# Kernel tuning notes

Measured on AMD Instinct MI355X. Metric: run time of the kernel, lower is better.

Reference implementation:

```python
import jax, jax.numpy as jnp
import numpy as np

EMBED_DIM = 1024
NUM_HEADS = 16
HEAD_DIM = EMBED_DIM // NUM_HEADS
GLOBAL_HEADS = 1
LOCAL_K = 128
SCALE = HEAD_DIM ** -0.5


def setup_inputs() -> dict:
    key = jax.random.key(0)
    ks = jax.random.split(key, 9)
    B, n = 4, 2048
    s = 1.0 / np.sqrt(EMBED_DIM)  # torch Linear default uniform(-1/sqrt(in), 1/sqrt(in))
    def lin(k):
        kw, kb = jax.random.split(k)
        W = jax.random.uniform(kw, (EMBED_DIM, EMBED_DIM), jnp.float32, -s, s)
        b = jax.random.uniform(kb, (EMBED_DIM,), jnp.float32, -s, s)
        return W, b
    wq, bq = lin(ks[0])
    wk, bk = lin(ks[1])
    wv, bv = lin(ks[2])
    wo, bo = lin(ks[3])
    x = jax.random.normal(ks[4], (B, n, EMBED_DIM), jnp.float32)
    return {"x": x, "wq": wq, "bq": bq, "wk": wk, "bk": bk,
            "wv": wv, "bv": bv, "wo": wo, "bo": bo}


def _attend(x, wq, bq, wk, bk, wv, bv, wo, bo):
    B, n, E = x.shape
    H, D = NUM_HEADS, HEAD_DIM
    def proj(W, b):
        t = x @ W.T + b                       # [B, n, E]
        return t.reshape(B, n, H, D).transpose(0, 2, 1, 3)  # [B, H, n, D]
    q, k, v = proj(wq, bq), proj(wk, bk), proj(wv, bv)
    scores = jnp.einsum('bhqd,bhkd->bhqk', q, k) * SCALE  # [B, H, n, n]
    idx = jnp.arange(n)
    band = jnp.abs(idx[:, None] - idx[None, :]) <= LOCAL_K  # [n, n] True = allowed
    is_global = jnp.arange(H) < GLOBAL_HEADS
    mask = band[None, :, :] | is_global[:, None, None]      # [H, n, n]
    scores = jnp.where(mask[None], scores, -jnp.inf)
    attn = jax.nn.softmax(scores, axis=-1)   # dropout is identity (p=0 / eval)
    out = jnp.einsum('bhqk,bhkd->bhqd', attn, v)
    out = out.transpose(0, 2, 1, 3).reshape(B, n, E)
    return out @ wo.T + bo


def reference(x, wq, bq, wk, bk, wv, bv, wo, bo):
    return _attend(x, wq, bq, wk, bk, wv, bv, wo, bo)
```

## Files before the change

kernel.cpp:

```cpp
#include <hip/hip_runtime.h>

typedef __attribute__((ext_vector_type(4))) float f32x4;
typedef __attribute__((ext_vector_type(8))) short s16x8;

#define GLDS(gsrc, ldst) \
  __builtin_amdgcn_global_load_lds((const __attribute__((address_space(1))) void*)(gsrc), \
                                   (__attribute__((address_space(3))) void*)(ldst), 16, 0, 0)

__device__ __forceinline__ ushort f2bf(float f) {
  union { float f; unsigned u; } x; x.f = f;
  unsigned r = (x.u + 0x7FFFu + ((x.u >> 16) & 1u)) >> 16;
  return (ushort)r;
}

__global__ __launch_bounds__(256) void castk(const float* __restrict__ in,
                                             ushort* __restrict__ outp, int n) {
  int i = (blockIdx.x * 256 + threadIdx.x) * 4;
  if (i >= n) return;
  float4 v = *(const float4*)(in + i);
  ushort4 r;
  r.x = f2bf(v.x); r.y = f2bf(v.y); r.z = f2bf(v.z); r.w = f2bf(v.w);
  *(ushort4*)(outp + i) = r;
}

__global__ __launch_bounds__(256) void castw(const float* __restrict__ w0, const float* __restrict__ w1,
                                             const float* __restrict__ w2, const float* __restrict__ w3,
                                             ushort* __restrict__ o0, ushort* __restrict__ o1,
                                             ushort* __restrict__ o2, ushort* __restrict__ o3) {
  int bid = blockIdx.x;
  int sel = bid >> 10;
  const float* in = (sel == 0) ? w0 : (sel == 1) ? w1 : (sel == 2) ? w2 : w3;
  ushort* outp    = (sel == 0) ? o0 : (sel == 1) ? o1 : (sel == 2) ? o2 : o3;
  int i = ((bid & 1023) * 256 + threadIdx.x) * 4;
  float4 v = *(const float4*)(in + i);
  ushort4 r;
  r.x = f2bf(v.x); r.y = f2bf(v.y); r.z = f2bf(v.z); r.w = f2bf(v.w);
  *(ushort4*)(outp + i) = r;
}

template<int OUTBF16>
__global__ __launch_bounds__(512, 2) void gemm256(
    const ushort* __restrict__ A, const ushort* __restrict__ Bt,
    const float* __restrict__ bias0, const float* __restrict__ bias1,
    const float* __restrict__ bias2,
    void* __restrict__ Cout, int M, int N, int K, int nxn)
{
  __shared__ __align__(16) ushort lds[73728];
  const int tid = threadIdx.x;
  const int w = tid >> 6, lane = tid & 63;
  const int lrow = lane & 15, lg = lane >> 4;
  const int wm = w >> 2, wn = w & 3;
  const int cpx = gridDim.x >> 3;
  const int wgid = ((int)blockIdx.x & 7) * cpx + ((int)blockIdx.x >> 3);
  const int mblk = (wgid / nxn) * 128;
  const int nblk = (wgid % nxn) * 256;
  const int NT = K >> 6;

  const int srow = tid >> 3;
  const int scol = 8 * ((tid & 7) ^ (srow & 7));
  const ushort* Abase = A + (size_t)(mblk + srow) * K + scol;
  const ushort* Bbase = Bt + (size_t)(nblk + srow) * K + scol;
  const size_t rstep = (size_t)64 * K;
  const int dA = w * 512;
  const int dB = 8192 + w * 512;

#define STAGE_A(kt, bf) { \
    GLDS(Abase + (size_t)(kt) * 64,         &lds[(bf) * 24576 + dA]); \
    GLDS(Abase + (size_t)(kt) * 64 + rstep, &lds[(bf) * 24576 + dA + 4096]); }
#define STAGE_B(kt, bf) { \
    GLDS(Bbase + (size_t)(kt) * 64,             &lds[(bf) * 24576 + dB]); \
    GLDS(Bbase + (size_t)(kt) * 64 + rstep,     &lds[(bf) * 24576 + dB + 4096]); \
    GLDS(Bbase + (size_t)(kt) * 64 + 2 * rstep, &lds[(bf) * 24576 + dB + 8192]); \
    GLDS(Bbase + (size_t)(kt) * 64 + 3 * rstep, &lds[(bf) * 24576 + dB + 12288]); }

  int offA[4][2], offB[4][2];
#pragma unroll
  for (int m = 0; m < 4; m++)
#pragma unroll
    for (int kk = 0; kk < 2; kk++) {
      offA[m][kk] = (wm * 64 + m * 16 + lrow) * 64 + (((kk * 4 + lg) ^ (lrow & 7)) << 3);
      offB[m][kk] = 8192 + (wn * 64 + m * 16 + lrow) * 64 + (((kk * 4 + lg) ^ (lrow & 7)) << 3);
    }

  const f32x4 zero = {0.f, 0.f, 0.f, 0.f};
  f32x4 acc[4][4];
#pragma unroll
  for (int m = 0; m < 4; m++)
#pragma unroll
    for (int n = 0; n < 4; n++) acc[m][n] = zero;

  STAGE_A(0, 0); STAGE_B(0, 0);
  if (NT > 1) { STAGE_A(1, 1); STAGE_B(1, 1); }

  int b = 0;
  for (int t = 0; t < NT; ++t) {
    if (t < NT - 1) { asm volatile("s_waitcnt vmcnt(6)" ::: "memory"); }
    else            { asm volatile("s_waitcnt vmcnt(0)" ::: "memory"); }
    __builtin_amdgcn_s_barrier();
    const int bb = b * 24576;
    const int t2 = t + 2;
    const int b2 = (b >= 1) ? b - 1 : 2;

    if (t2 < NT) STAGE_A(t2, b2);
    {
      s16x8 af[4], bf_[4];
#pragma unroll
      for (int m = 0; m < 4; m++) af[m] = *(const s16x8*)&lds[bb + offA[m][0]];
#pragma unroll
      for (int n = 0; n < 4; n++) bf_[n] = *(const s16x8*)&lds[bb + offB[n][0]];
      __builtin_amdgcn_s_setprio(1);
#pragma unroll
      for (int m = 0; m < 4; m++)
#pragma unroll
        for (int n = 0; n < 4; n++)
          acc[m][n] = __builtin_amdgcn_mfma_f32_16x16x32_bf16(af[m], bf_[n], acc[m][n], 0, 0, 0);
      __builtin_amdgcn_s_setprio(0);
    }
    if (t2 < NT) STAGE_B(t2, b2);
    {
      s16x8 af[4], bf_[4];
#pragma unroll
      for (int m = 0; m < 4; m++) af[m] = *(const s16x8*)&lds[bb + offA[m][1]];
#pragma unroll
      for (int n = 0; n < 4; n++) bf_[n] = *(const s16x8*)&lds[bb + offB[n][1]];
      __builtin_amdgcn_s_setprio(1);
#pragma unroll
      for (int m = 0; m < 4; m++)
#pragma unroll
        for (int n = 0; n < 4; n++)
          acc[m][n] = __builtin_amdgcn_mfma_f32_16x16x32_bf16(af[m], bf_[n], acc[m][n], 0, 0, 0);
      __builtin_amdgcn_s_setprio(0);
    }
    b = (b == 2) ? 0 : b + 1;
  }
#undef STAGE_A
#undef STAGE_B

  float bias_n[4];
#pragma unroll
  for (int n = 0; n < 4; n++) {
    const int col = nblk + wn * 64 + n * 16 + lrow;
    if (bias1) bias_n[n] = (col < 1024) ? bias0[col]
                          : (col < 2048 ? bias1[col - 1024] : bias2[col - 2048]);
    else bias_n[n] = bias0[col];
  }

  __syncthreads();

  if (OUTBF16) {
    ushort* Ct = lds;
#pragma unroll
    for (int m = 0; m < 4; m++)
#pragma unroll
      for (int n = 0; n < 4; n++)
#pragma unroll
        for (int i = 0; i < 4; i++)
          Ct[(wm * 64 + m * 16 + 4 * lg + i) * 256 + wn * 64 + n * 16 + lrow] =
              f2bf(acc[m][n][i] + bias_n[n]);
    __syncthreads();
    ushort* Cg = (ushort*)Cout;
#pragma unroll
    for (int r = 0; r < 8; r++) {
      const int row = r * 16 + (tid >> 5);
      const int col = (tid & 31) * 8;
      *(s16x8*)&Cg[(size_t)(mblk + row) * N + nblk + col] = *(const s16x8*)&lds[r * 4096 + tid * 8];
    }
  } else {
    float* Cf = (float*)lds;
#pragma unroll
    for (int m = 0; m < 4; m++)
#pragma unroll
      for (int n = 0; n < 4; n++)
#pragma unroll
        for (int i = 0; i < 4; i++)
          Cf[(wm * 64 + m * 16 + 4 * lg + i) * 256 + wn * 64 + n * 16 + lrow] =
              acc[m][n][i] + bias_n[n];
    __syncthreads();
    float* Cg = (float*)Cout;
#pragma unroll
    for (int r = 0; r < 16; r++) {
      const int row = r * 8 + (tid >> 6);
      const int col = (tid & 63) * 4;
      *(float4*)&Cg[(size_t)(mblk + row) * N + nblk + col] = *(const float4*)&Cf[r * 2048 + tid * 4];
    }
  }
}

__global__ __launch_bounds__(256) void attn_kernel(const ushort* __restrict__ qkv,
                                                   ushort* __restrict__ outp,
                                                   float* __restrict__ oPart,
                                                   float* __restrict__ mPart,
                                                   float* __restrict__ lPart)
{
  __shared__ __align__(16) ushort Ks[64 * 64];
  __shared__ __align__(16) ushort Vt[64 * 64];
  __shared__ __align__(16) ushort Ps[4][16 * 40];

  const int tid = threadIdx.x;
  const int w = tid >> 6, lane = tid & 63;
  const int lrow = lane & 15, lg = lane >> 4;

  const int bid = (blockIdx.x & 7) * 368 + (blockIdx.x >> 3);
  int h, b, bx, kv_lo, kv_hi, chunk = 0;
  bool isGlobal;
  if (bid < 1024) {
    isGlobal = true; h = 0;
    chunk = bid >> 7;
    int qb = bid & 127;
    b = qb >> 5; bx = qb & 31;
    kv_lo = chunk * 256; kv_hi = kv_lo + 256;
  } else {
    isGlobal = false;
    int t = bid - 1024;
    h = 1 + (t >> 7);
    int qb = t & 127;
    b = qb >> 5; bx = qb & 31;
    kv_lo = bx * 64 - 128; if (kv_lo < 0) kv_lo = 0;
    kv_hi = bx * 64 + 192; if (kv_hi > 2048) kv_hi = 2048;
  }
  const int q0b = bx * 64;
  const int q0 = q0b + w * 16;
  const ushort* Qp = qkv + (size_t)b * 2048 * 3072 + h * 64;
  const ushort* Kp = Qp + 1024;
  const ushort* Vp = Qp + 2048;

  s16x8 qf0 = *(const s16x8*)(Qp + (size_t)(q0 + lrow) * 3072 + 8 * lg);
  s16x8 qf1 = *(const s16x8*)(Qp + (size_t)(q0 + lrow) * 3072 + 32 + 8 * lg);

  const f32x4 zero = {0.f, 0.f, 0.f, 0.f};
  f32x4 o[4];
  o[0] = zero; o[1] = zero; o[2] = zero; o[3] = zero;
  float mrun = -3e38f, lsum = 0.f;
  const int q_abs = q0 + lrow;
  const float SCL = 0.18033688011112042f;

  const int sp = tid >> 3;
  const int sg = tid & 7;
  const int kr0 = tid >> 3;
  const int kc = tid & 7;
  const int vx = (lrow & 7) ^ (lrow >> 3);

  for (int kv = kv_lo; kv < kv_hi; kv += 64) {
    const bool needMask = !isGlobal && (kv < q0b - 64 || kv + 64 > q0b + 128);

    const ushort* vrow = Vp + (size_t)(kv + 2 * sp) * 3072 + 8 * sg;
    s16x8 vlo = *(const s16x8*)vrow;
    s16x8 vhi = *(const s16x8*)(vrow + 3072);

    __syncthreads();

    GLDS(Kp + (size_t)(kv + kr0) * 3072 + 8 * (kc ^ (kr0 & 7)), &Ks[w * 512]);
    GLDS(Kp + (size_t)(kv + 32 + kr0) * 3072 + 8 * (kc ^ (kr0 & 7)), &Ks[2048 + w * 512]);

#pragma unroll
    for (int j = 0; j < 8; j++) {
      const int d = 8 * sg + j;
      const int r = 2 * sp;
      uint pk = (uint)(ushort)vlo[j] | ((uint)(ushort)vhi[j] << 16);
      *(uint*)&Vt[d * 64 + ((((r >> 3) ^ j ^ sg) & 7) << 3) + (r & 7)] = pk;
    }
    __syncthreads();

#pragma unroll
    for (int s = 0; s < 2; s++) {
      const int kb = kv + 32 * s;
      const int rs = 32 * s;
      s16x8 kA0 = *(const s16x8*)&Ks[(rs + lrow) * 64      + ((( lg      ^ (lrow & 7)) & 7) << 3)];
      s16x8 kA1 = *(const s16x8*)&Ks[(rs + lrow) * 64      + ((((4 + lg) ^ (lrow & 7)) & 7) << 3)];
      s16x8 kB0 = *(const s16x8*)&Ks[(rs + 16 + lrow) * 64 + ((( lg      ^ (lrow & 7)) & 7) << 3)];
      s16x8 kB1 = *(const s16x8*)&Ks[(rs + 16 + lrow) * 64 + ((((4 + lg) ^ (lrow & 7)) & 7) << 3)];

      f32x4 sA = __builtin_amdgcn_mfma_f32_16x16x32_bf16(kA0, qf0, zero, 0, 0, 0);
      sA = __builtin_amdgcn_mfma_f32_16x16x32_bf16(kA1, qf1, sA, 0, 0, 0);
      f32x4 sB = __builtin_amdgcn_mfma_f32_16x16x32_bf16(kB0, qf0, zero, 0, 0, 0);
      sB = __builtin_amdgcn_mfma_f32_16x16x32_bf16(kB1, qf1, sB, 0, 0, 0);

      float pA[4], pB[4];
      float rowmax = -3e38f;
      if (needMask) {
#pragma unroll
        for (int i = 0; i < 4; i++) {
          int kaA = kb + 4 * lg + i;
          int dq = q_abs - kaA;
          float va = (dq <= 128 && dq >= -128) ? sA[i] * SCL : -1e30f;
          pA[i] = va; rowmax = fmaxf(rowmax, va);
          int dqb = dq - 16;
          float vb = (dqb <= 128 && dqb >= -128) ? sB[i] * SCL : -1e30f;
          pB[i] = vb; rowmax = fmaxf(rowmax, vb);
        }
      } else {
#pragma unroll
        for (int i = 0; i < 4; i++) {
          pA[i] = sA[i] * SCL; pB[i] = sB[i] * SCL;
          rowmax = fmaxf(rowmax, fmaxf(pA[i], pB[i]));
        }
      }
      rowmax = fmaxf(rowmax, __shfl_xor(rowmax, 16));
      rowmax = fmaxf(rowmax, __shfl_xor(rowmax, 32));

      if (!__all(rowmax <= mrun + 8.f)) {
        float mnew = fmaxf(mrun, rowmax);
        float alpha = exp2f(mrun - mnew);
        mrun = mnew;
        lsum *= alpha;
        float a0 = __shfl(alpha, 4 * lg + 0);
        float a1 = __shfl(alpha, 4 * lg + 1);
        float a2 = __shfl(alpha, 4 * lg + 2);
        float a3 = __shfl(alpha, 4 * lg + 3);
#pragma unroll
        for (int c = 0; c < 4; c++) {
          o[c][0] *= a0; o[c][1] *= a1; o[c][2] *= a2; o[c][3] *= a3;
        }
      }

      float rsum = 0.f;
      if (needMask) {
#pragma unroll
        for (int i = 0; i < 4; i++) {
          pA[i] = (pA[i] > -1e29f) ? exp2f(pA[i] - mrun) : 0.f;
          pB[i] = (pB[i] > -1e29f) ? exp2f(pB[i] - mrun) : 0.f;
          rsum += pA[i] + pB[i];
        }
      } else {
#pragma unroll
        for (int i = 0; i < 4; i++) {
          pA[i] = exp2f(pA[i] - mrun);
          pB[i] = exp2f(pB[i] - mrun);
          rsum += pA[i] + pB[i];
        }
      }
      rsum += __shfl_xor(rsum, 16);
      rsum += __shfl_xor(rsum, 32);
      lsum += rsum;

      {
        ushort* P = &Ps[w][lrow * 40];
        *(uint*)&P[4 * lg]      = (uint)f2bf(pA[0]) | ((uint)f2bf(pA[1]) << 16);
        *(uint*)&P[4 * lg + 2]  = (uint)f2bf(pA[2]) | ((uint)f2bf(pA[3]) << 16);
        *(uint*)&P[16 + 4 * lg] = (uint)f2bf(pB[0]) | ((uint)f2bf(pB[1]) << 16);
        *(uint*)&P[18 + 4 * lg] = (uint)f2bf(pB[2]) | ((uint)f2bf(pB[3]) << 16);
      }
      s16x8 paf = *(const s16x8*)&Ps[w][lrow * 40 + 8 * lg];

#pragma unroll
      for (int c = 0; c < 4; c++) {
        const int d = 16 * c + lrow;
        s16x8 vf = *(const s16x8*)&Vt[d * 64 + ((((4 * s + lg) ^ vx ^ (2 * c)) & 7) << 3)];
        o[c] = __builtin_amdgcn_mfma_f32_16x16x32_bf16(paf, vf, o[c], 0, 0, 0);
      }
    }
  }

  if (isGlobal) {
    const size_t rbase = (size_t)(chunk * 4 + b) * 2048 + q0;
    if (lg == 0) {
      mPart[rbase + lrow] = mrun;
      lPart[rbase + lrow] = lsum;
    }
#pragma unroll
    for (int c = 0; c < 4; c++)
#pragma unroll
      for (int i = 0; i < 4; i++)
        oPart[(rbase + 4 * lg + i) * 64 + 16 * c + lrow] = o[c][i];
  } else {
    float li0 = 1.f / __shfl(lsum, 4 * lg + 0);
    float li1 = 1.f / __shfl(lsum, 4 * lg + 1);
    float li2 = 1.f / __shfl(lsum, 4 * lg + 2);
    float li3 = 1.f / __shfl(lsum, 4 * lg + 3);
    size_t orow = (size_t)(b * 2048 + q0 + 4 * lg);
#pragma unroll
    for (int c = 0; c < 4; c++) {
      outp[(orow + 0) * 1024 + h * 64 + 16 * c + lrow] = f2bf(o[c][0] * li0);
      outp[(orow + 1) * 1024 + h * 64 + 16 * c + lrow] = f2bf(o[c][1] * li1);
      outp[(orow + 2) * 1024 + h * 64 + 16 * c + lrow] = f2bf(o[c][2] * li2);
      outp[(orow + 3) * 1024 + h * 64 + 16 * c + lrow] = f2bf(o[c][3] * li3);
    }
  }
}

__global__ __launch_bounds__(256) void combine_kernel(const float* __restrict__ oPart,
                                                      const float* __restrict__ mPart,
                                                      const float* __restrict__ lPart,
                                                      ushort* __restrict__ attno) {
  const int tid = threadIdx.x;
  const int row = blockIdx.x * 64 + (tid >> 2);
  const int d0 = (tid & 3) * 16;
  float m[8], l[8], M = -3e38f;
#pragma unroll
  for (int p = 0; p < 8; p++) {
    m[p] = mPart[p * 8192 + row];
    l[p] = lPart[p * 8192 + row];
    M = fmaxf(M, m[p]);
  }
  float L = 0.f, wgt[8];
#pragma unroll
  for (int p = 0; p < 8; p++) { wgt[p] = exp2f(m[p] - M); L += wgt[p] * l[p]; }
  float inv = 1.f / L;
  float acc[16];
#pragma unroll
  for (int j = 0; j < 16; j++) acc[j] = 0.f;
#pragma unroll
  for (int p = 0; p < 8; p++) {
    const float* op = oPart + ((size_t)p * 8192 + row) * 64 + d0;
    float wv = wgt[p];
#pragma unroll
    for (int j = 0; j < 16; j += 4) {
      float4 v = *(const float4*)(op + j);
      acc[j]     += wv * v.x; acc[j + 1] += wv * v.y;
      acc[j + 2] += wv * v.z; acc[j + 3] += wv * v.w;
    }
  }
  ushort* dst = attno + (size_t)row * 1024 + d0;
#pragma unroll
  for (int j = 0; j < 16; j++) dst[j] = f2bf(acc[j] * inv);
}

extern "C" void kernel_launch(void* const* d_in, const int* in_sizes, int n_in,
                              void* d_out, int out_size, void* d_ws, size_t ws_size,
                              hipStream_t stream) {
  const float* x  = (const float*)d_in[0];
  const float* wq = (const float*)d_in[1];
  const float* bq = (const float*)d_in[2];
  const float* wk = (const float*)d_in[3];
  const float* bk = (const float*)d_in[4];
  const float* wv = (const float*)d_in[5];
  const float* bv = (const float*)d_in[6];
  const float* wo = (const float*)d_in[7];
  const float* bo = (const float*)d_in[8];

  char* ws = (char*)d_ws;
  ushort* xb    = (ushort*)(ws);
  ushort* wqkvb = (ushort*)(ws + 16777216);
  ushort* wob   = (ushort*)(ws + 23068672);
  ushort* qkvb  = (ushort*)(ws + 25165824);
  ushort* attno = (ushort*)(ws + 75497472);
  float* oPart = (float*)(ws);
  float* mPart = (float*)(ws + 16777216);
  float* lPart = (float*)(ws + 16777216 + 262144);

  castk<<<8192, 256, 0, stream>>>(x, xb, 8388608);
  castw<<<4096, 256, 0, stream>>>(wq, wk, wv, wo,
                                  wqkvb, wqkvb + 1048576, wqkvb + 2097152, wob);

  gemm256<1><<<768, 512, 0, stream>>>(xb, wqkvb, bq, bk, bv,
                                      (void*)qkvb, 8192, 3072, 1024, 12);

  attn_kernel<<<2944, 256, 0, stream>>>(qkvb, attno, oPart, mPart, lPart);
  combine_kernel<<<128, 256, 0, stream>>>(oPart, mPart, lPart, attno);

  gemm256<0><<<256, 512, 0, stream>>>(attno, wob, bo, nullptr, nullptr,
                                      (void*)d_out, 8192, 1024, 1024, 4);
}
```

Before: 167.1 us.

## Replace GEMM with templated double-buffered 8-phase pipelined kernel and retile QKV projection

Replaces the triple-buffered 128x256 GEMM with a templated kernel that double-buffers LDS and splits each K-tile into barrier-separated phases, issuing the next tile's global-to-LDS loads in the middle of the MFMA work. The QKV projection now uses 256x192 tiles over 512 blocks, and the output projection keeps 128x256 tiles. The fp32 epilogue is written out in two halves to fit the smaller LDS. The goal is better overlap of loads with MFMA and less LDS use. In exchange it adds more barriers per iteration and has only two buffers to hide load latency.

```diff
diff --git a/kernel.cpp b/kernel.cpp
--- a/kernel.cpp
+++ b/kernel.cpp
@@ -11,6 +11,13 @@
   union { float f; unsigned u; } x; x.f = f;
   unsigned r = (x.u + 0x7FFFu + ((x.u >> 16) & 1u)) >> 16;
   return (ushort)r;
+}
+
+template<int N> __device__ __forceinline__ void waitvm() {
+  if constexpr (N == 0) asm volatile("s_waitcnt vmcnt(0)" ::: "memory");
+  else if constexpr (N == 6) asm volatile("s_waitcnt vmcnt(6)" ::: "memory");
+  else if constexpr (N == 7) asm volatile("s_waitcnt vmcnt(7)" ::: "memory");
+  else if constexpr (N == 8) asm volatile("s_waitcnt vmcnt(8)" ::: "memory");
 }
 
 __global__ __launch_bounds__(256) void castk(const float* __restrict__ in,
@@ -38,150 +45,218 @@
   *(ushort4*)(outp + i) = r;
 }
 
-template<int OUTBF16>
-__global__ __launch_bounds__(512, 2) void gemm256(
+template<int MREP, int NREP, int OUTBF16>
+__global__ __launch_bounds__(512) void gemm8p(
     const ushort* __restrict__ A, const ushort* __restrict__ Bt,
     const float* __restrict__ bias0, const float* __restrict__ bias1,
     const float* __restrict__ bias2,
     void* __restrict__ Cout, int M, int N, int K, int nxn)
 {
-  __shared__ __align__(16) ushort lds[73728];
+  constexpr int BM = 32 * MREP;
+  constexpr int BN = 64 * NREP;
+  constexpr int AUS = BM * 64;
+  constexpr int SBUF = (BM + BN) * 64;
+  constexpr int IA = BM / 64;
+  constexpr int IB = BN / 64;
+  constexpr int TOT = IA + IB;
+
+  __shared__ __align__(16) ushort lds[2 * SBUF];
+
   const int tid = threadIdx.x;
   const int w = tid >> 6, lane = tid & 63;
   const int lrow = lane & 15, lg = lane >> 4;
   const int wm = w >> 2, wn = w & 3;
   const int cpx = gridDim.x >> 3;
   const int wgid = ((int)blockIdx.x & 7) * cpx + ((int)blockIdx.x >> 3);
-  const int mblk = (wgid / nxn) * 128;
-  const int nblk = (wgid % nxn) * 256;
+  const int mblk = (wgid / nxn) * BM;
+  const int nblk = (wgid % nxn) * BN;
   const int NT = K >> 6;
 
   const int srow = tid >> 3;
-  const int scol = 8 * ((tid & 7) ^ (srow & 7));
-  const ushort* Abase = A + (size_t)(mblk + srow) * K + scol;
-  const ushort* Bbase = Bt + (size_t)(nblk + srow) * K + scol;
+  const int sg8 = 8 * ((tid & 7) ^ (srow & 7));
+  const ushort* Ab = A + (size_t)(mblk + srow) * K + sg8;
+  const ushort* Bb = Bt + (size_t)(nblk + srow) * K + sg8;
   const size_t rstep = (size_t)64 * K;
-  const int dA = w * 512;
-  const int dB = 8192 + w * 512;
-
-#define STAGE_A(kt, bf) { \
-    GLDS(Abase + (size_t)(kt) * 64,         &lds[(bf) * 24576 + dA]); \
-    GLDS(Abase + (size_t)(kt) * 64 + rstep, &lds[(bf) * 24576 + dA + 4096]); }
-#define STAGE_B(kt, bf) { \
-    GLDS(Bbase + (size_t)(kt) * 64,             &lds[(bf) * 24576 + dB]); \
-    GLDS(Bbase + (size_t)(kt) * 64 + rstep,     &lds[(bf) * 24576 + dB + 4096]); \
-    GLDS(Bbase + (size_t)(kt) * 64 + 2 * rstep, &lds[(bf) * 24576 + dB + 8192]); \
-    GLDS(Bbase + (size_t)(kt) * 64 + 3 * rstep, &lds[(bf) * 24576 + dB + 12288]); }
-
-  int offA[4][2], offB[4][2];
-#pragma unroll
-  for (int m = 0; m < 4; m++)
-#pragma unroll
-    for (int kk = 0; kk < 2; kk++) {
-      offA[m][kk] = (wm * 64 + m * 16 + lrow) * 64 + (((kk * 4 + lg) ^ (lrow & 7)) << 3);
-      offB[m][kk] = 8192 + (wn * 64 + m * 16 + lrow) * 64 + (((kk * 4 + lg) ^ (lrow & 7)) << 3);
-    }
+
+  auto stageA = [&](const ushort* p, int dst) {
+#pragma unroll
+    for (int R = 0; R < IA; R++)
+      GLDS(p + (size_t)R * rstep, &lds[dst + R * 4096 + w * 512]);
+  };
+  auto stageB = [&](const ushort* p, int dst) {
+#pragma unroll
+    for (int R = 0; R < IB; R++)
+      GLDS(p + (size_t)R * rstep, &lds[dst + AUS + R * 4096 + w * 512]);
+  };
+
+  const int xs0 = (lg ^ (lrow & 7)) << 3;
+  const int xs1 = ((4 + lg) ^ (lrow & 7)) << 3;
+  const int laneA0 = (wm * (BM / 2) + lrow) * 64 + xs0;
+  const int laneA1 = (wm * (BM / 2) + lrow) * 64 + xs1;
+  const int laneB0 = AUS + (wn * (16 * NREP) + lrow) * 64 + xs0;
+  const int laneB1 = AUS + (wn * (16 * NREP) + lrow) * 64 + xs1;
 
   const f32x4 zero = {0.f, 0.f, 0.f, 0.f};
-  f32x4 acc[4][4];
-#pragma unroll
-  for (int m = 0; m < 4; m++)
-#pragma unroll
-    for (int n = 0; n < 4; n++) acc[m][n] = zero;
-
-  STAGE_A(0, 0); STAGE_B(0, 0);
-  if (NT > 1) { STAGE_A(1, 1); STAGE_B(1, 1); }
-
-  int b = 0;
+  f32x4 acc[MREP][NREP];
+#pragma unroll
+  for (int m = 0; m < MREP; m++)
+#pragma unroll
+    for (int n = 0; n < NREP; n++) acc[m][n] = zero;
+
+  stageA(Ab, 0);       stageB(Bb, 0);
+  stageA(Ab + 64, SBUF); stageB(Bb + 64, SBUF);
+  const ushort* aN = Ab + 128;
+  const ushort* bN = Bb + 128;
+
+  int bb = 0;
   for (int t = 0; t < NT; ++t) {
-    if (t < NT - 1) { asm volatile("s_waitcnt vmcnt(6)" ::: "memory"); }
-    else            { asm volatile("s_waitcnt vmcnt(0)" ::: "memory"); }
+    if (t < NT - 1) waitvm<TOT>(); else waitvm<0>();
     __builtin_amdgcn_s_barrier();
-    const int bb = b * 24576;
-    const int t2 = t + 2;
-    const int b2 = (b >= 1) ? b - 1 : 2;
-
-    if (t2 < NT) STAGE_A(t2, b2);
-    {
-      s16x8 af[4], bf_[4];
-#pragma unroll
-      for (int m = 0; m < 4; m++) af[m] = *(const s16x8*)&lds[bb + offA[m][0]];
-#pragma unroll
-      for (int n = 0; n < 4; n++) bf_[n] = *(const s16x8*)&lds[bb + offB[n][0]];
+    const bool pf = (t + 2 < NT);
+
+    if constexpr (MREP == 8) {
+      s16x8 af[4], bfr[NREP];
+#pragma unroll
+      for (int j = 0; j < 4; j++) af[j] = *(const s16x8*)&lds[bb + laneA0 + j * 1024];
+#pragma unroll
+      for (int n = 0; n < NREP; n++) bfr[n] = *(const s16x8*)&lds[bb + laneB0 + n * 1024];
+      __builtin_amdgcn_s_barrier();
       __builtin_amdgcn_s_setprio(1);
 #pragma unroll
-      for (int m = 0; m < 4; m++)
-#pragma unroll
-        for (int n = 0; n < 4; n++)
-          acc[m][n] = __builtin_amdgcn_mfma_f32_16x16x32_bf16(af[m], bf_[n], acc[m][n], 0, 0, 0);
+      for (int j = 0; j < 4; j++)
+#pragma unroll
+        for (int n = 0; n < NREP; n++)
+          acc[j][n] = __builtin_amdgcn_mfma_f32_16x16x32_bf16(af[j], bfr[n], acc[j][n], 0, 0, 0);
       __builtin_amdgcn_s_setprio(0);
-    }
-    if (t2 < NT) STAGE_B(t2, b2);
-    {
-      s16x8 af[4], bf_[4];
-#pragma unroll
-      for (int m = 0; m < 4; m++) af[m] = *(const s16x8*)&lds[bb + offA[m][1]];
-#pragma unroll
-      for (int n = 0; n < 4; n++) bf_[n] = *(const s16x8*)&lds[bb + offB[n][1]];
+      __builtin_amdgcn_s_barrier();
+#pragma unroll
+      for (int j = 0; j < 4; j++) af[j] = *(const s16x8*)&lds[bb + laneA0 + (4 + j) * 1024];
+      __builtin_amdgcn_s_barrier();
       __builtin_amdgcn_s_setprio(1);
 #pragma unroll
-      for (int m = 0; m < 4; m++)
-#pragma unroll
-        for (int n = 0; n < 4; n++)
-          acc[m][n] = __builtin_amdgcn_mfma_f32_16x16x32_bf16(af[m], bf_[n], acc[m][n], 0, 0, 0);
+      for (int j = 0; j < 4; j++)
+#pragma unroll
+        for (int n = 0; n < NREP; n++)
+          acc[4 + j][n] = __builtin_amdgcn_mfma_f32_16x16x32_bf16(af[j], bfr[n], acc[4 + j][n], 0, 0, 0);
       __builtin_amdgcn_s_setprio(0);
-    }
-    b = (b == 2) ? 0 : b + 1;
-  }
-#undef STAGE_A
-#undef STAGE_B
-
-  float bias_n[4];
-#pragma unroll
-  for (int n = 0; n < 4; n++) {
-    const int col = nblk + wn * 64 + n * 16 + lrow;
+      __builtin_amdgcn_s_barrier();
+#pragma unroll
+      for (int j = 0; j < 4; j++) af[j] = *(const s16x8*)&lds[bb + laneA1 + j * 1024];
+#pragma unroll
+      for (int n = 0; n < NREP; n++) bfr[n] = *(const s16x8*)&lds[bb + laneB1 + n * 1024];
+      __builtin_amdgcn_s_barrier();
+      if (pf) stageB(bN, bb);
+      __builtin_amdgcn_s_setprio(1);
+#pragma unroll
+      for (int j = 0; j < 4; j++)
+#pragma unroll
+        for (int n = 0; n < NREP; n++)
+          acc[j][n] = __builtin_amdgcn_mfma_f32_16x16x32_bf16(af[j], bfr[n], acc[j][n], 0, 0, 0);
+      __builtin_amdgcn_s_setprio(0);
+      __builtin_amdgcn_s_barrier();
+#pragma unroll
+      for (int j = 0; j < 4; j++) af[j] = *(const s16x8*)&lds[bb + laneA1 + (4 + j) * 1024];
+      __builtin_amdgcn_s_barrier();
+      if (pf) stageA(aN, bb);
+      __builtin_amdgcn_s_setprio(1);
+#pragma unroll
+      for (int j = 0; j < 4; j++)
+#pragma unroll
+        for (int n = 0; n < NREP; n++)
+          acc[4 + j][n] = __builtin_amdgcn_mfma_f32_16x16x32_bf16(af[j], bfr[n], acc[4 + j][n], 0, 0, 0);
+      __builtin_amdgcn_s_setprio(0);
+    } else {
+      s16x8 af[4], bfr[NREP];
+#pragma unroll
+      for (int j = 0; j < 4; j++) af[j] = *(const s16x8*)&lds[bb + laneA0 + j * 1024];
+#pragma unroll
+      for (int n = 0; n < NREP; n++) bfr[n] = *(const s16x8*)&lds[bb + laneB0 + n * 1024];
+      __builtin_amdgcn_s_barrier();
+      __builtin_amdgcn_s_setprio(1);
+#pragma unroll
+      for (int j = 0; j < 4; j++)
+#pragma unroll
+        for (int n = 0; n < NREP; n++)
+          acc[j][n] = __builtin_amdgcn_mfma_f32_16x16x32_bf16(af[j], bfr[n], acc[j][n], 0, 0, 0);
+      __builtin_amdgcn_s_setprio(0);
+      __builtin_amdgcn_s_barrier();
+#pragma unroll
+      for (int j = 0; j < 4; j++) af[j] = *(const s16x8*)&lds[bb + laneA1 + j * 1024];
+#pragma unroll
+      for (int n = 0; n < NREP; n++) bfr[n] = *(const s16x8*)&lds[bb + laneB1 + n * 1024];
+      __builtin_amdgcn_s_barrier();
+      if (pf) { stageA(aN, bb); stageB(bN, bb); }
+      __builtin_amdgcn_s_setprio(1);
+#pragma unroll
+      for (int j = 0; j < 4; j++)
+#pragma unroll
+        for (int n = 0; n < NREP; n++)
+          acc[j][n] = __builtin_amdgcn_mfma_f32_16x16x32_bf16(af[j], bfr[n], acc[j][n], 0, 0, 0);
+      __builtin_amdgcn_s_setprio(0);
+    }
+
+    if (pf) { aN += 64; bN += 64; }
+    bb ^= SBUF;
+  }
+
+  float bias_n[NREP];
+#pragma unroll
+  for (int n = 0; n < NREP; n++) {
+    const int col = nblk + wn * (16 * NREP) + n * 16 + lrow;
     if (bias1) bias_n[n] = (col < 1024) ? bias0[col]
                           : (col < 2048 ? bias1[col - 1024] : bias2[col - 2048]);
     else bias_n[n] = bias0[col];
   }
 
-  __syncthreads();
-
-  if (OUTBF16) {
+  if constexpr (OUTBF16) {
+    __syncthreads();
     ushort* Ct = lds;
 #pragma unroll
-    for (int m = 0; m < 4; m++)
-#pragma unroll
-      for (int n = 0; n < 4; n++)
+    for (int m = 0; m < MREP; m++)
+#pragma unroll
+      for (int n = 0; n < NREP; n++) {
+        f32x4 v = acc[m][n];
 #pragma unroll
         for (int i = 0; i < 4; i++)
-          Ct[(wm * 64 + m * 16 + 4 * lg + i) * 256 + wn * 64 + n * 16 + lrow] =
-              f2bf(acc[m][n][i] + bias_n[n]);
+          Ct[(wm * (BM / 2) + m * 16 + 4 * lg + i) * BN + wn * (16 * NREP) + n * 16 + lrow] =
+              f2bf(v[i] + bias_n[n]);
+      }
     __syncthreads();
     ushort* Cg = (ushort*)Cout;
-#pragma unroll
-    for (int r = 0; r < 8; r++) {
-      const int row = r * 16 + (tid >> 5);
-      const int col = (tid & 31) * 8;
-      *(s16x8*)&Cg[(size_t)(mblk + row) * N + nblk + col] = *(const s16x8*)&lds[r * 4096 + tid * 8];
+    constexpr int GR = BM * BN / 8;
+#pragma unroll
+    for (int p = 0; p < GR / 512; p++) {
+      unsigned g = p * 512 + tid;
+      unsigned row = g / (BN / 8);
+      unsigned cg = g % (BN / 8);
+      *(s16x8*)&Cg[(size_t)(mblk + row) * N + nblk + cg * 8] = *(const s16x8*)&lds[g * 8];
     }
   } else {
     float* Cf = (float*)lds;
-#pragma unroll
-    for (int m = 0; m < 4; m++)
-#pragma unroll
-      for (int n = 0; n < 4; n++)
-#pragma unroll
-        for (int i = 0; i < 4; i++)
-          Cf[(wm * 64 + m * 16 + 4 * lg + i) * 256 + wn * 64 + n * 16 + lrow] =
-              acc[m][n][i] + bias_n[n];
-    __syncthreads();
     float* Cg = (float*)Cout;
 #pragma unroll
-    for (int r = 0; r < 16; r++) {
-      const int row = r * 8 + (tid >> 6);
-      const int col = (tid & 63) * 4;
-      *(float4*)&Cg[(size_t)(mblk + row) * N + nblk + col] = *(const float4*)&Cf[r * 2048 + tid * 4];
+    for (int ch = 0; ch < 2; ch++) {
+      __syncthreads();
+      if (wm == ch) {
+#pragma unroll
+        for (int m = 0; m < MREP; m++)
+#pragma unroll
+          for (int n = 0; n < NREP; n++) {
+            f32x4 v = acc[m][n];
+#pragma unroll
+            for (int i = 0; i < 4; i++)
+              Cf[(m * 16 + 4 * lg + i) * BN + wn * (16 * NREP) + n * 16 + lrow] = v[i] + bias_n[n];
+          }
+      }
+      __syncthreads();
+#pragma unroll
+      for (int p = 0; p < (64 * BN / 4) / 512; p++) {
+        unsigned fg = p * 512 + tid;
+        unsigned row = fg / (BN / 4);
+        unsigned c4 = fg % (BN / 4);
+        *(float4*)&Cg[(size_t)(mblk + ch * 64 + row) * N + nblk + c4 * 4] =
+            *(const float4*)&Cf[row * BN + c4 * 4];
+      }
     }
   }
 }
@@ -442,12 +517,12 @@
   castw<<<4096, 256, 0, stream>>>(wq, wk, wv, wo,
                                   wqkvb, wqkvb + 1048576, wqkvb + 2097152, wob);
 
-  gemm256<1><<<768, 512, 0, stream>>>(xb, wqkvb, bq, bk, bv,
-                                      (void*)qkvb, 8192, 3072, 1024, 12);
+  gemm8p<8, 3, 1><<<512, 512, 0, stream>>>(xb, wqkvb, bq, bk, bv,
+                                           (void*)qkvb, 8192, 3072, 1024, 16);
 
   attn_kernel<<<2944, 256, 0, stream>>>(qkvb, attno, oPart, mPart, lPart);
   combine_kernel<<<128, 256, 0, stream>>>(oPart, mPart, lPart, attno);
 
-  gemm256<0><<<256, 512, 0, stream>>>(attno, wob, bo, nullptr, nullptr,
-                                      (void*)d_out, 8192, 1024, 1024, 4);
-}
+  gemm8p<4, 4, 0><<<256, 512, 0, stream>>>(attno, wob, bo, nullptr, nullptr,
+                                           (void*)d_out, 8192, 1024, 1024, 4);
+}
```

Result: faster. 161.4 us (-3.4%).
